# Kernel optimization log

Measured on AMD Instinct MI355X. Metric: run time of the kernel, lower is better.

## Reference

```python
import jax, jax.numpy as jnp
import numpy as np

N, E = 100000, 3200000
IN, HID, OUT, EDGE = 32, 32, 32, 8

def _lin(k, fi, fo):
    s = 1.0 / np.sqrt(fi)
    return jax.random.uniform(k, (fi, fo), jnp.float32, -s, s)

def setup_inputs() -> dict:
    key = jax.random.key(0)
    ks = jax.random.split(key, 12)
    return {
        "node_feat": jax.random.normal(ks[0], (N, IN), jnp.float32),
        "coord_feat": jax.random.normal(ks[1], (N, 3), jnp.float32),
        "edge_feat": jax.random.normal(ks[2], (E, EDGE), jnp.float32),
        "src": jax.random.randint(ks[3], (E,), 0, N, jnp.int32),
        "dst": jax.random.randint(ks[4], (E,), 0, N, jnp.int32),
        # edge MLP: Linear(2*IN+EDGE+1 -> HID), SiLU, Linear(HID -> HID), SiLU
        "We1": _lin(ks[5], 2 * IN + EDGE + 1, HID), "be1": jnp.zeros((HID,), jnp.float32),
        "We2": _lin(ks[6], HID, HID), "be2": jnp.zeros((HID,), jnp.float32),
        # node MLP: Linear(IN+HID -> HID), SiLU, Linear(HID -> OUT)
        "Wn1": _lin(ks[7], IN + HID, HID), "bn1": jnp.zeros((HID,), jnp.float32),
        "Wn2": _lin(ks[8], HID, OUT), "bn2": jnp.zeros((OUT,), jnp.float32),
        # coord MLP: Linear(HID -> HID), SiLU, Linear(HID -> 1, bias=False)
        "Wc1": _lin(ks[9], HID, HID), "bc1": jnp.zeros((HID,), jnp.float32),
        "Wc2": _lin(ks[10], HID, 1),
    }

def reference(node_feat, coord_feat, edge_feat, src, dst,
              We1, be1, We2, be2, Wn1, bn1, Wn2, bn2, Wc1, bc1, Wc2):
    silu = jax.nn.silu
    # per-edge coordinate difference and radial feature (DGL EGNNConv math)
    x_diff = coord_feat[src] - coord_feat[dst]                       # [E,3]
    radial = jnp.sum(x_diff * x_diff, axis=-1, keepdims=True)        # [E,1]
    x_diff = x_diff / (jnp.sqrt(radial) + 1e-30)                     # normalized
    # edge MLP on concat(src_h, dst_h, radial, edge_feat)
    f = jnp.concatenate([node_feat[src], node_feat[dst], radial, edge_feat], axis=-1)
    msg_h = silu(silu(f @ We1 + be1) @ We2 + be2)                    # [E,HID]
    # coordinate message (coord MLP scalar gate * normalized diff)
    msg_x = (silu(msg_h @ Wc1 + bc1) @ Wc2) * x_diff                 # [E,3]
    # aggregate: sum for h messages, mean for coord messages (at dst)
    h_neigh = jax.ops.segment_sum(msg_h, dst, num_segments=N)        # [N,HID]
    deg = jax.ops.segment_sum(jnp.ones((E, 1), msg_x.dtype), dst, num_segments=N)
    x_neigh = jax.ops.segment_sum(msg_x, dst, num_segments=N) / jnp.maximum(deg, 1.0)
    # node update
    h = silu(jnp.concatenate([node_feat, h_neigh], axis=-1) @ Wn1 + bn1) @ Wn2 + bn2
    x = coord_feat + x_neigh
    return h, x
```

## Files before the change

### kernel.cpp

```cpp
#include <hip/hip_runtime.h>
#include <math.h>

#define TIN   32
#define THID  32
#define TOUT  32
#define TEDGE 8
#define CHUNK 4
#define MAXDEG 64

typedef __attribute__((ext_vector_type(8))) short bf16x8;
typedef __attribute__((ext_vector_type(4))) float f32x4;

#define MFMA16(a, b, c) __builtin_amdgcn_mfma_f32_16x16x32_bf16((a), (b), (c), 0, 0, 0)

__device__ __forceinline__ unsigned int cvtpk(float lo, float hi) {
    unsigned int r;
    asm("v_cvt_pk_bf16_f32 %0, %1, %2" : "=v"(r) : "v"(lo), "v"(hi));
    return r;
}

__device__ __forceinline__ float silu_f(float x) {
    float e = __expf(-x);
    return x * __builtin_amdgcn_rcpf(1.0f + e);
}

union U4F { unsigned int u[4]; bf16x8 v; };
union U4Q { uint4 q; bf16x8 v; };

__device__ __forceinline__ bf16x8 pack8bf(const float* f) {
    U4F t;
    t.u[0] = cvtpk(f[0], f[1]);
    t.u[1] = cvtpk(f[2], f[3]);
    t.u[2] = cvtpk(f[4], f[5]);
    t.u[3] = cvtpk(f[6], f[7]);
    return t.v;
}

__device__ __forceinline__ bf16x8 load_wT(const float* __restrict__ W, int kbase, int ch, int Kreal) {
    float f[8];
    #pragma unroll
    for (int e = 0; e < 8; ++e) {
        int k = kbase + e;
        f[e] = (k < Kreal) ? W[k * 32 + ch] : 0.0f;
    }
    return pack8bf(f);
}

__device__ __forceinline__ bf16x8 load_wA12(const float* __restrict__ We1,
                                            const float* __restrict__ be1, int g, int ch) {
    float f[8];
    #pragma unroll
    for (int e = 0; e < 8; ++e) f[e] = 0.0f;
    if (g == 0) { f[0] = We1[64 * 32 + ch]; f[1] = be1[ch]; }
    else if (g == 1) {
        #pragma unroll
        for (int e = 0; e < 8; ++e) f[e] = We1[(65 + e) * 32 + ch];
    }
    return pack8bf(f);
}

__global__ __launch_bounds__(256) void conv_node_kernel(
    const float* __restrict__ nf, unsigned int* __restrict__ nb, int total )
{
    int i = blockIdx.x * 256 + threadIdx.x;
    int stride = gridDim.x * 256;
    for (; i < total; i += stride) {
        float2 v = reinterpret_cast<const float2*>(nf)[i];
        nb[i] = cvtpk(v.x, v.y);
    }
}

__global__ __launch_bounds__(256) void conv_coord_kernel(
    const float* __restrict__ c, float4* __restrict__ c4, int N)
{
    int i = blockIdx.x * 256 + threadIdx.x;
    int stride = gridDim.x * 256;
    for (; i < N; i += stride) {
        float4 v;
        v.x = c[3*(size_t)i+0]; v.y = c[3*(size_t)i+1]; v.z = c[3*(size_t)i+2]; v.w = 0.0f;
        c4[i] = v;
    }
}

__global__ __launch_bounds__(256) void record_rank_kernel(
    const int* __restrict__ src,
    const int* __restrict__ dst,
    const float* __restrict__ edge_feat,
    int* __restrict__ cnt,
    int* __restrict__ srcA,
    uint4* __restrict__ efA,
    int E)
{
    int e = blockIdx.x * 256 + threadIdx.x;
    if (e >= E) return;
    int d = dst[e];
    int rank = atomicAdd(&cnt[d], 1);
    if (rank >= MAXDEG) return;
    int slot = (d << 6) + rank;

    srcA[slot] = src[e];
    const float4* ep = reinterpret_cast<const float4*>(edge_feat + (size_t)e * TEDGE);
    float4 e0 = ep[0], e1 = ep[1];
    uint4 ef;
    ef.x = cvtpk(e0.x, e0.y);
    ef.y = cvtpk(e0.z, e0.w);
    ef.z = cvtpk(e1.x, e1.y);
    ef.w = cvtpk(e1.z, e1.w);
    efA[slot] = ef;
}

__global__ __launch_bounds__(256) void egnn_fused(
    const uint4* __restrict__ node_bf4,
    const float4* __restrict__ coord4,
    const int*  __restrict__ srcA,
    const uint4* __restrict__ efA,
    const int*  __restrict__ cnt,
    const float* __restrict__ We1,
    const float* __restrict__ be1,
    const float* __restrict__ We2,
    const float* __restrict__ be2,
    const float* __restrict__ Wc1,
    const float* __restrict__ bc1,
    const float* __restrict__ Wc2,
    float4* __restrict__ h_acc4,
    float4* __restrict__ xd4,
    int N)
{
    const int lane = threadIdx.x & 63;
    const int wid  = threadIdx.x >> 6;
    const int r    = lane & 15;
    const int g    = lane >> 4;

    bf16x8 A10[2], A11[2], A12[2], A2[2], A3[2];
    A10[0] = load_wT(We1,      8*g, r,      73);
    A10[1] = load_wT(We1,      8*g, 16 + r, 73);
    A11[0] = load_wT(We1, 32 + 8*g, r,      73);
    A11[1] = load_wT(We1, 32 + 8*g, 16 + r, 73);
    A12[0] = load_wA12(We1, be1, g, r);
    A12[1] = load_wA12(We1, be1, g, 16 + r);
    A2[0] = load_wT(We2, 8*g, r, 32);      A2[1] = load_wT(We2, 8*g, 16 + r, 32);
    A3[0] = load_wT(Wc1, 8*g, r, 32);      A3[1] = load_wT(Wc1, 8*g, 16 + r, 32);

    float be2v[8], bc1v[8], wc2v[8];
    #pragma unroll
    for (int h = 0; h < 2; ++h)
        #pragma unroll
        for (int q = 0; q < 4; ++q) {
            int ch = 16*h + 4*g + q;
            be2v[4*h+q] = be2[ch];
            bc1v[4*h+q] = bc1[ch];
            wc2v[4*h+q] = Wc2[ch];
        }

    const bool Hhi = ((g >> 1) & 1) != 0;
    const int  s0L = 32 * (g & 1) + r;
    const int  s1L = s0L + 16;

    int c0n = (blockIdx.x * 4 + wid) * CHUNK;

    for (int n = c0n; n < c0n + CHUNK && n < N; ++n) {
        int deg = cnt[n];
        int len = deg < MAXDEG ? deg : MAXDEG;
        int segbase = n << 6;

        U4Q Bd; Bd.q = node_bf4[(size_t)n * 4 + g];
        float4 cd = coord4[n];

        f32x4 z4 = {0.f,0.f,0.f,0.f};
        f32x4 dst0 = MFMA16(A11[0], Bd.v, z4);
        f32x4 dst1 = MFMA16(A11[1], Bd.v, z4);

        float ha0[4] = {0.f,0.f,0.f,0.f}, ha1[4] = {0.f,0.f,0.f,0.f};
        float xa0 = 0.f, xa1 = 0.f, xa2 = 0.f;

        for (int t = 0; t < len; t += 16) {
            int idx = t + r;
            bool valid = idx < len;
            int slot = segbase + (valid ? idx : 0);

            int srcv = srcA[slot];
            U4Q Bs; Bs.q = node_bf4[(size_t)srcv * 4 + g];

            float dx0 = 0.f, dx1 = 0.f, dx2 = 0.f;
            U4F Bk2;
            Bk2.u[0] = 0u; Bk2.u[1] = 0u; Bk2.u[2] = 0u; Bk2.u[3] = 0u;
            if (g == 0) {
                float4 cs = coord4[srcv];
                dx0 = cs.x - cd.x; dx1 = cs.y - cd.y; dx2 = cs.z - cd.z;
                float radial = dx0*dx0 + dx1*dx1 + dx2*dx2;
                float invn = __builtin_amdgcn_rcpf(sqrtf(radial) + 1e-30f);
                dx0 *= invn; dx1 *= invn; dx2 *= invn;
                Bk2.u[0] = cvtpk(radial, 1.0f);
            } else if (g == 1) {
                uint4 ef = efA[slot];
                Bk2.u[0] = ef.x; Bk2.u[1] = ef.y; Bk2.u[2] = ef.z; Bk2.u[3] = ef.w;
            }

            f32x4 acc0 = dst0, acc1 = dst1;
            acc0 = MFMA16(A10[0], Bs.v,   acc0);
            acc0 = MFMA16(A12[0], Bk2.v,  acc0);
            acc1 = MFMA16(A10[1], Bs.v,   acc1);
            acc1 = MFMA16(A12[1], Bk2.v,  acc1);

            unsigned int pk0 = cvtpk(silu_f(acc0[0]), silu_f(acc0[1]));
            unsigned int pk1 = cvtpk(silu_f(acc0[2]), silu_f(acc0[3]));
            unsigned int pk2 = cvtpk(silu_f(acc1[0]), silu_f(acc1[1]));
            unsigned int pk3 = cvtpk(silu_f(acc1[2]), silu_f(acc1[3]));

            unsigned int al0 = __shfl(pk0, s0L, 64), al1 = __shfl(pk1, s0L, 64);
            unsigned int ah0 = __shfl(pk2, s0L, 64), ah1 = __shfl(pk3, s0L, 64);
            unsigned int bl0 = __shfl(pk0, s1L, 64), bl1 = __shfl(pk1, s1L, 64);
            unsigned int bh0 = __shfl(pk2, s1L, 64), bh1 = __shfl(pk3, s1L, 64);
            U4F B2u;
            B2u.u[0] = Hhi ? ah0 : al0;  B2u.u[1] = Hhi ? ah1 : al1;
            B2u.u[2] = Hhi ? bh0 : bl0;  B2u.u[3] = Hhi ? bh1 : bl1;

            f32x4 m0, m1;
            #pragma unroll
            for (int q = 0; q < 4; ++q) { m0[q] = be2v[q]; m1[q] = be2v[4+q]; }
            m0 = MFMA16(A2[0], B2u.v, m0);
            m1 = MFMA16(A2[1], B2u.v, m1);

            float vm = valid ? 1.0f : 0.0f;
            float s00 = silu_f(m0[0]) * vm, s01 = silu_f(m0[1]) * vm;
            float s02 = silu_f(m0[2]) * vm, s03 = silu_f(m0[3]) * vm;
            float s10 = silu_f(m1[0]) * vm, s11 = silu_f(m1[1]) * vm;
            float s12 = silu_f(m1[2]) * vm, s13 = silu_f(m1[3]) * vm;

            ha0[0] += s00; ha0[1] += s01; ha0[2] += s02; ha0[3] += s03;
            ha1[0] += s10; ha1[1] += s11; ha1[2] += s12; ha1[3] += s13;

            unsigned int mpk0 = cvtpk(s00, s01);
            unsigned int mpk1 = cvtpk(s02, s03);
            unsigned int mpk2 = cvtpk(s10, s11);
            unsigned int mpk3 = cvtpk(s12, s13);

            unsigned int cl0 = __shfl(mpk0, s0L, 64), cl1 = __shfl(mpk1, s0L, 64);
            unsigned int ch0 = __shfl(mpk2, s0L, 64), ch1 = __shfl(mpk3, s0L, 64);
            unsigned int dl0 = __shfl(mpk0, s1L, 64), dl1 = __shfl(mpk1, s1L, 64);
            unsigned int dh0 = __shfl(mpk2, s1L, 64), dh1 = __shfl(mpk3, s1L, 64);
            U4F B3u;
            B3u.u[0] = Hhi ? ch0 : cl0;  B3u.u[1] = Hhi ? ch1 : cl1;
            B3u.u[2] = Hhi ? dh0 : dl0;  B3u.u[3] = Hhi ? dh1 : dl1;

            f32x4 c0, c1;
            #pragma unroll
            for (int q = 0; q < 4; ++q) { c0[q] = bc1v[q]; c1[q] = bc1v[4+q]; }
            c0 = MFMA16(A3[0], B3u.v, c0);
            c1 = MFMA16(A3[1], B3u.v, c1);

            float gp = 0.0f;
            #pragma unroll
            for (int q = 0; q < 4; ++q) {
                gp = fmaf(silu_f(c0[q]), wc2v[q],   gp);
                gp = fmaf(silu_f(c1[q]), wc2v[4+q], gp);
            }
            gp += __shfl_xor(gp, 16, 64);
            gp += __shfl_xor(gp, 32, 64);

            xa0 = fmaf(gp * vm, dx0, xa0);
            xa1 = fmaf(gp * vm, dx1, xa1);
            xa2 = fmaf(gp * vm, dx2, xa2);
        }

        #pragma unroll
        for (int off = 1; off < 16; off <<= 1) {
            #pragma unroll
            for (int q = 0; q < 4; ++q) {
                ha0[q] += __shfl_xor(ha0[q], off, 64);
                ha1[q] += __shfl_xor(ha1[q], off, 64);
            }
            xa0 += __shfl_xor(xa0, off, 64);
            xa1 += __shfl_xor(xa1, off, 64);
            xa2 += __shfl_xor(xa2, off, 64);
        }

        if (r == 0) {
            float4 v0; v0.x = ha0[0]; v0.y = ha0[1]; v0.z = ha0[2]; v0.w = ha0[3];
            float4 v1; v1.x = ha1[0]; v1.y = ha1[1]; v1.z = ha1[2]; v1.w = ha1[3];
            h_acc4[(size_t)n * 8 + g]     = v0;
            h_acc4[(size_t)n * 8 + 4 + g] = v1;
            if (g == 0) {
                float4 xv; xv.x = xa0; xv.y = xa1; xv.z = xa2; xv.w = (float)deg;
                xd4[n] = xv;
            }
        }
    }
}

__global__ __launch_bounds__(256) void ovf_fix_node(
    const float* __restrict__ node_feat,
    const float* __restrict__ coord,
    const float* __restrict__ edge_feat,
    const int* __restrict__ src,
    const int* __restrict__ dst,
    const int* __restrict__ cnt,
    const float* __restrict__ We1,
    const float* __restrict__ be1,
    const float* __restrict__ We2,
    const float* __restrict__ be2,
    const float* __restrict__ Wc1,
    const float* __restrict__ bc1,
    const float* __restrict__ Wc2,
    float* __restrict__ h_acc,
    float4* __restrict__ xd4,
    int N, int E)
{
    int n = blockIdx.x * 256 + threadIdx.x;
    if (n >= N) return;
    if (cnt[n] <= MAXDEG) return;

    float hsum[THID];
    #pragma unroll
    for (int j = 0; j < THID; ++j) hsum[j] = 0.f;
    float xs0 = 0.f, xs1 = 0.f, xs2 = 0.f;
    int degc = 0;
    for (int ee = 0; ee < E; ++ee) {
        if (dst[ee] != n) continue;
        ++degc;
        int ss = src[ee];
        float dx0 = coord[3*(size_t)ss+0] - coord[3*(size_t)n+0];
        float dx1 = coord[3*(size_t)ss+1] - coord[3*(size_t)n+1];
        float dx2 = coord[3*(size_t)ss+2] - coord[3*(size_t)n+2];
        float radial = dx0*dx0 + dx1*dx1 + dx2*dx2;
        float invn = 1.0f / (sqrtf(radial) + 1e-30f);
        dx0 *= invn; dx1 *= invn; dx2 *= invn;
        float f[73];
        for (int k = 0; k < 32; ++k) f[k] = node_feat[(size_t)ss*TIN + k];
        for (int k = 0; k < 32; ++k) f[32+k] = node_feat[(size_t)n*TIN + k];
        f[64] = radial;
        for (int k = 0; k < 8; ++k) f[65+k] = edge_feat[(size_t)ee*TEDGE + k];
        float a1[THID];
        for (int j = 0; j < THID; ++j) a1[j] = be1[j];
        for (int k = 0; k < 73; ++k) {
            float fk = f[k];
            for (int j = 0; j < THID; ++j) a1[j] = fmaf(fk, We1[k*THID + j], a1[j]);
        }
        for (int j = 0; j < THID; ++j) a1[j] = silu_f(a1[j]);
        float msg[THID];
        for (int j = 0; j < THID; ++j) msg[j] = be2[j];
        for (int k = 0; k < THID; ++k) {
            float fk = a1[k];
            for (int j = 0; j < THID; ++j) msg[j] = fmaf(fk, We2[k*THID + j], msg[j]);
        }
        for (int j = 0; j < THID; ++j) msg[j] = silu_f(msg[j]);
        float c1[THID];
        for (int j = 0; j < THID; ++j) c1[j] = bc1[j];
        for (int k = 0; k < THID; ++k) {
            float fk = msg[k];
            for (int j = 0; j < THID; ++j) c1[j] = fmaf(fk, Wc1[k*THID + j], c1[j]);
        }
        float gate = 0.0f;
        for (int j = 0; j < THID; ++j) gate = fmaf(silu_f(c1[j]), Wc2[j], gate);
        for (int j = 0; j < THID; ++j) hsum[j] += msg[j];
        xs0 += gate * dx0; xs1 += gate * dx1; xs2 += gate * dx2;
    }
    for (int j = 0; j < THID; ++j) h_acc[(size_t)n * THID + j] = hsum[j];
    float4 xv; xv.x = xs0; xv.y = xs1; xv.z = xs2; xv.w = (float)degc;
    xd4[n] = xv;
}

__global__ __launch_bounds__(256) void egnn_edge_atomic(
    const float* __restrict__ node_feat,
    const float* __restrict__ coord,
    const float* __restrict__ edge_feat,
    const int*   __restrict__ src,
    const int*   __restrict__ dst,
    const float* __restrict__ We1,
    const float* __restrict__ be1,
    const float* __restrict__ We2,
    const float* __restrict__ be2,
    const float* __restrict__ Wc1,
    const float* __restrict__ bc1,
    const float* __restrict__ Wc2,
    float* __restrict__ h_acc,
    float* __restrict__ x_acc,
    int E)
{
    int e = blockIdx.x * 256 + threadIdx.x;
    if (e >= E) return;
    int s = src[e];
    int d = dst[e];
    float dx0 = coord[3*(size_t)s+0] - coord[3*(size_t)d+0];
    float dx1 = coord[3*(size_t)s+1] - coord[3*(size_t)d+1];
    float dx2 = coord[3*(size_t)s+2] - coord[3*(size_t)d+2];
    float radial = dx0*dx0 + dx1*dx1 + dx2*dx2;
    float invn = 1.0f / (sqrtf(radial) + 1e-30f);
    dx0 *= invn; dx1 *= invn; dx2 *= invn;
    float f[73];
    #pragma unroll
    for (int i = 0; i < 32; ++i) f[i] = node_feat[(size_t)s*TIN + i];
    #pragma unroll
    for (int i = 0; i < 32; ++i) f[32+i] = node_feat[(size_t)d*TIN + i];
    f[64] = radial;
    #pragma unroll
    for (int i = 0; i < 8; ++i) f[65+i] = edge_feat[(size_t)e*TEDGE + i];
    float a1[THID];
    #pragma unroll
    for (int j = 0; j < THID; ++j) a1[j] = be1[j];
    for (int k = 0; k < 73; ++k) {
        float fk = f[k];
        #pragma unroll
        for (int j = 0; j < THID; ++j) a1[j] = fmaf(fk, We1[k*THID + j], a1[j]);
    }
    #pragma unroll
    for (int j = 0; j < THID; ++j) a1[j] = silu_f(a1[j]);
    float msg[THID];
    #pragma unroll
    for (int j = 0; j < THID; ++j) msg[j] = be2[j];
    for (int k = 0; k < THID; ++k) {
        float fk = a1[k];
        #pragma unroll
        for (int j = 0; j < THID; ++j) msg[j] = fmaf(fk, We2[k*THID + j], msg[j]);
    }
    #pragma unroll
    for (int j = 0; j < THID; ++j) msg[j] = silu_f(msg[j]);
    float c1[THID];
    #pragma unroll
    for (int j = 0; j < THID; ++j) c1[j] = bc1[j];
    for (int k = 0; k < THID; ++k) {
        float fk = msg[k];
        #pragma unroll
        for (int j = 0; j < THID; ++j) c1[j] = fmaf(fk, Wc1[k*THID + j], c1[j]);
    }
    float gate = 0.0f;
    #pragma unroll
    for (int j = 0; j < THID; ++j) gate = fmaf(silu_f(c1[j]), Wc2[j], gate);
    float* ha = h_acc + (size_t)d * THID;
    #pragma unroll
    for (int j = 0; j < THID; ++j) atomicAdd(ha + j, msg[j]);
    atomicAdd(x_acc + (size_t)d*4 + 0, gate * dx0);
    atomicAdd(x_acc + (size_t)d*4 + 1, gate * dx1);
    atomicAdd(x_acc + (size_t)d*4 + 2, gate * dx2);
    atomicAdd(x_acc + (size_t)d*4 + 3, 1.0f);
}

__global__ __launch_bounds__(256) void egnn_node(
    const float* __restrict__ node_feat,
    const float* __restrict__ coord,
    const float* __restrict__ Wn1,
    const float* __restrict__ bn1,
    const float* __restrict__ Wn2,
    const float* __restrict__ bn2,
    const float* __restrict__ h_acc,
    const float4* __restrict__ xd4,
    float* __restrict__ out_h,
    float* __restrict__ out_x,
    int N)
{
    int n = blockIdx.x * 256 + threadIdx.x;
    if (n >= N) return;

    float f2[2*TIN];
    {
        const float4* p = reinterpret_cast<const float4*>(node_feat + (size_t)n * TIN);
        #pragma unroll
        for (int i = 0; i < TIN/4; ++i) {
            float4 v = p[i];
            f2[4*i+0]=v.x; f2[4*i+1]=v.y; f2[4*i+2]=v.z; f2[4*i+3]=v.w;
        }
    }
    {
        const float4* p = reinterpret_cast<const float4*>(h_acc + (size_t)n * THID);
        #pragma unroll
        for (int i = 0; i < THID/4; ++i) {
            float4 v = p[i];
            f2[TIN+4*i+0]=v.x; f2[TIN+4*i+1]=v.y; f2[TIN+4*i+2]=v.z; f2[TIN+4*i+3]=v.w;
        }
    }

    float a[THID];
    #pragma unroll
    for (int j = 0; j < THID; ++j) a[j] = bn1[j];
    #pragma unroll
    for (int k = 0; k < 2*TIN; ++k) {
        float fk = f2[k];
        #pragma unroll
        for (int j = 0; j < THID; ++j) a[j] = fmaf(fk, Wn1[k*THID + j], a[j]);
    }
    #pragma unroll
    for (int j = 0; j < THID; ++j) a[j] = silu_f(a[j]);

    float h[TOUT];
    #pragma unroll
    for (int j = 0; j < TOUT; ++j) h[j] = bn2[j];
    #pragma unroll
    for (int k = 0; k < THID; ++k) {
        float fk = a[k];
        #pragma unroll
        for (int j = 0; j < TOUT; ++j) h[j] = fmaf(fk, Wn2[k*TOUT + j], h[j]);
    }

    float4* po = reinterpret_cast<float4*>(out_h + (size_t)n * TOUT);
    #pragma unroll
    for (int i = 0; i < TOUT/4; ++i) {
        float4 v; v.x=h[4*i+0]; v.y=h[4*i+1]; v.z=h[4*i+2]; v.w=h[4*i+3];
        po[i] = v;
    }

    float4 xv = xd4[n];
    float dg = fmaxf(xv.w, 1.0f);
    float inv = __builtin_amdgcn_rcpf(dg);
    out_x[(size_t)n*3+0] = coord[(size_t)n*3+0] + xv.x * inv;
    out_x[(size_t)n*3+1] = coord[(size_t)n*3+1] + xv.y * inv;
    out_x[(size_t)n*3+2] = coord[(size_t)n*3+2] + xv.z * inv;
}

extern "C" void kernel_launch(void* const* d_in, const int* in_sizes, int n_in,
                              void* d_out, int out_size, void* d_ws, size_t ws_size,
                              hipStream_t stream) {
    const float* node_feat = (const float*)d_in[0];
    const float* coord     = (const float*)d_in[1];
    const float* edge_feat = (const float*)d_in[2];
    const int*   src       = (const int*)d_in[3];
    const int*   dst       = (const int*)d_in[4];
    const float* We1 = (const float*)d_in[5];
    const float* be1 = (const float*)d_in[6];
    const float* We2 = (const float*)d_in[7];
    const float* be2 = (const float*)d_in[8];
    const float* Wn1 = (const float*)d_in[9];
    const float* bn1 = (const float*)d_in[10];
    const float* Wn2 = (const float*)d_in[11];
    const float* bn2 = (const float*)d_in[12];
    const float* Wc1 = (const float*)d_in[13];
    const float* bc1 = (const float*)d_in[14];
    const float* Wc2 = (const float*)d_in[15];

    int N = in_sizes[0] / TIN;
    int E = in_sizes[3];

    float* out_h = (float*)d_out;
    float* out_x = out_h + (size_t)N * TOUT;

    uint4*        efA     = (uint4*)d_ws;
    float4*       coord4  = (float4*)(efA + ((size_t)N << 6));
    float4*       xd4     = coord4 + N;
    float*        h_acc   = (float*)(xd4 + N);
    unsigned int* node_bf = (unsigned int*)(h_acc + (size_t)N * THID);
    int*          srcA    = (int*)(node_bf + (size_t)N * 16);
    int*          cnt     = srcA + ((size_t)N << 6);
    size_t need = (size_t)((char*)(cnt + N + 1) - (char*)d_ws);

    if (need <= ws_size) {
        conv_node_kernel<<<2048, 256, 0, stream>>>(node_feat, node_bf, N * 16);
        conv_coord_kernel<<<(N + 255) / 256, 256, 0, stream>>>(coord, coord4, N);
        hipMemsetAsync(cnt, 0, (size_t)(N + 1) * 4, stream);
        record_rank_kernel<<<(E + 255) / 256, 256, 0, stream>>>(
            src, dst, edge_feat, cnt, srcA, efA, E);
        int nchunks = (N + CHUNK - 1) / CHUNK;
        egnn_fused<<<(nchunks + 3) / 4, 256, 0, stream>>>(
            (const uint4*)node_bf, coord4, srcA, efA, cnt,
            We1, be1, We2, be2, Wc1, bc1, Wc2,
            (float4*)h_acc, xd4, N);
        ovf_fix_node<<<(N + 255) / 256, 256, 0, stream>>>(
            node_feat, coord, edge_feat, src, dst, cnt,
            We1, be1, We2, be2, Wc1, bc1, Wc2, h_acc, xd4, N, E);
        egnn_node<<<(N + 255) / 256, 256, 0, stream>>>(
            node_feat, coord, Wn1, bn1, Wn2, bn2,
            h_acc, xd4, out_h, out_x, N);
    } else {
        float* fh_acc = (float*)d_ws;
        float* fx_acc = fh_acc + (size_t)N * THID;
        hipMemsetAsync(d_ws, 0, sizeof(float) * (size_t)N * (THID + 4), stream);
        egnn_edge_atomic<<<(E + 255) / 256, 256, 0, stream>>>(
            node_feat, coord, edge_feat, src, dst,
            We1, be1, We2, be2, Wc1, bc1, Wc2,
            fh_acc, fx_acc, E);
        egnn_node<<<(N + 255) / 256, 256, 0, stream>>>(
            node_feat, coord, Wn1, bn1, Wn2, bn2,
            fh_acc, (const float4*)fx_acc, out_h, out_x, N);
    }
}
```

Baseline: 520.0 us.

## Precompute per-edge geometry in rank kernel and pack into 32-byte edge records

After: 476.4 us. 8.4% less time.

```diff
diff --git a/kernel.cpp b/kernel.cpp
--- a/kernel.cpp
+++ b/kernel.cpp
@@ -23,6 +23,9 @@
     float e = __expf(-x);
     return x * __builtin_amdgcn_rcpf(1.0f + e);
 }
+
+__device__ __forceinline__ float bflo(unsigned int u) { return __uint_as_float(u << 16); }
+__device__ __forceinline__ float bfhi(unsigned int u) { return __uint_as_float(u & 0xFFFF0000u); }
 
 union U4F { unsigned int u[4]; bf16x8 v; };
 union U4Q { uint4 q; bf16x8 v; };
@@ -51,10 +54,10 @@
     float f[8];
     #pragma unroll
     for (int e = 0; e < 8; ++e) f[e] = 0.0f;
-    if (g == 0) { f[0] = We1[64 * 32 + ch]; f[1] = be1[ch]; }
+    if (g == 0) { f[0] = We1[72 * 32 + ch]; f[1] = be1[ch]; }
     else if (g == 1) {
         #pragma unroll
-        for (int e = 0; e < 8; ++e) f[e] = We1[(65 + e) * 32 + ch];
+        for (int e = 0; e < 8; ++e) f[e] = We1[(64 + e) * 32 + ch];
     }
     return pack8bf(f);
 }
@@ -85,35 +88,45 @@
 __global__ __launch_bounds__(256) void record_rank_kernel(
     const int* __restrict__ src,
     const int* __restrict__ dst,
+    const float4* __restrict__ coord4,
     const float* __restrict__ edge_feat,
     int* __restrict__ cnt,
-    int* __restrict__ srcA,
-    uint4* __restrict__ efA,
+    uint4* __restrict__ recs,
     int E)
 {
     int e = blockIdx.x * 256 + threadIdx.x;
     if (e >= E) return;
-    int d = dst[e];
+    int s = src[e], d = dst[e];
     int rank = atomicAdd(&cnt[d], 1);
     if (rank >= MAXDEG) return;
-    int slot = (d << 6) + rank;
-
-    srcA[slot] = src[e];
+
+    float4 cs = coord4[s];
+    float4 cd = coord4[d];
+    float dx0 = cs.x - cd.x, dx1 = cs.y - cd.y, dx2 = cs.z - cd.z;
+    float radial = dx0*dx0 + dx1*dx1 + dx2*dx2;
+    float invn = __builtin_amdgcn_rcpf(sqrtf(radial) + 1e-30f);
+    dx0 *= invn; dx1 *= invn; dx2 *= invn;
+
     const float4* ep = reinterpret_cast<const float4*>(edge_feat + (size_t)e * TEDGE);
     float4 e0 = ep[0], e1 = ep[1];
-    uint4 ef;
-    ef.x = cvtpk(e0.x, e0.y);
-    ef.y = cvtpk(e0.z, e0.w);
-    ef.z = cvtpk(e1.x, e1.y);
-    ef.w = cvtpk(e1.z, e1.w);
-    efA[slot] = ef;
+
+    size_t slot = ((size_t)d << 6) + rank;
+    uint4 r0, r1;
+    r0.x = (unsigned int)s;
+    r0.y = cvtpk(dx0, dx1);
+    r0.z = cvtpk(dx2, e1.w);
+    r0.w = 0u;
+    r1.x = cvtpk(radial, e0.x);
+    r1.y = cvtpk(e0.y, e0.z);
+    r1.z = cvtpk(e0.w, e1.x);
+    r1.w = cvtpk(e1.y, e1.z);
+    recs[2*slot + 0] = r0;
+    recs[2*slot + 1] = r1;
 }
 
 __global__ __launch_bounds__(256) void egnn_fused(
     const uint4* __restrict__ node_bf4,
-    const float4* __restrict__ coord4,
-    const int*  __restrict__ srcA,
-    const uint4* __restrict__ efA,
+    const uint4* __restrict__ recs,
     const int*  __restrict__ cnt,
     const float* __restrict__ We1,
     const float* __restrict__ be1,
@@ -161,10 +174,9 @@
     for (int n = c0n; n < c0n + CHUNK && n < N; ++n) {
         int deg = cnt[n];
         int len = deg < MAXDEG ? deg : MAXDEG;
-        int segbase = n << 6;
+        size_t segbase = ((size_t)n << 6);
 
         U4Q Bd; Bd.q = node_bf4[(size_t)n * 4 + g];
-        float4 cd = coord4[n];
 
         f32x4 z4 = {0.f,0.f,0.f,0.f};
         f32x4 dst0 = MFMA16(A11[0], Bd.v, z4);
@@ -176,24 +188,19 @@
         for (int t = 0; t < len; t += 16) {
             int idx = t + r;
             bool valid = idx < len;
-            int slot = segbase + (valid ? idx : 0);
-
-            int srcv = srcA[slot];
+            size_t slot = segbase + (valid ? idx : 0);
+
+            uint4 rc = recs[2*slot + (g & 1)];
+            int srcv = __shfl((int)rc.x, r, 64);
+
             U4Q Bs; Bs.q = node_bf4[(size_t)srcv * 4 + g];
 
-            float dx0 = 0.f, dx1 = 0.f, dx2 = 0.f;
             U4F Bk2;
             Bk2.u[0] = 0u; Bk2.u[1] = 0u; Bk2.u[2] = 0u; Bk2.u[3] = 0u;
             if (g == 0) {
-                float4 cs = coord4[srcv];
-                dx0 = cs.x - cd.x; dx1 = cs.y - cd.y; dx2 = cs.z - cd.z;
-                float radial = dx0*dx0 + dx1*dx1 + dx2*dx2;
-                float invn = __builtin_amdgcn_rcpf(sqrtf(radial) + 1e-30f);
-                dx0 *= invn; dx1 *= invn; dx2 *= invn;
-                Bk2.u[0] = cvtpk(radial, 1.0f);
+                Bk2.u[0] = (rc.z >> 16) | 0x3F800000u;
             } else if (g == 1) {
-                uint4 ef = efA[slot];
-                Bk2.u[0] = ef.x; Bk2.u[1] = ef.y; Bk2.u[2] = ef.z; Bk2.u[3] = ef.w;
+                Bk2.u[0] = rc.x; Bk2.u[1] = rc.y; Bk2.u[2] = rc.z; Bk2.u[3] = rc.w;
             }
 
             f32x4 acc0 = dst0, acc1 = dst1;
@@ -258,9 +265,10 @@
             gp += __shfl_xor(gp, 16, 64);
             gp += __shfl_xor(gp, 32, 64);
 
-            xa0 = fmaf(gp * vm, dx0, xa0);
-            xa1 = fmaf(gp * vm, dx1, xa1);
-            xa2 = fmaf(gp * vm, dx2, xa2);
+            float xd0 = bflo(rc.y), xd1 = bfhi(rc.y), xd2 = bflo(rc.z);
+            xa0 = fmaf(gp * vm, xd0, xa0);
+            xa1 = fmaf(gp * vm, xd1, xa1);
+            xa2 = fmaf(gp * vm, xd2, xa2);
         }
 
         #pragma unroll
@@ -532,13 +540,12 @@
     float* out_h = (float*)d_out;
     float* out_x = out_h + (size_t)N * TOUT;
 
-    uint4*        efA     = (uint4*)d_ws;
-    float4*       coord4  = (float4*)(efA + ((size_t)N << 6));
-    float4*       xd4     = coord4 + N;
-    float*        h_acc   = (float*)(xd4 + N);
-    unsigned int* node_bf = (unsigned int*)(h_acc + (size_t)N * THID);
-    int*          srcA    = (int*)(node_bf + (size_t)N * 16);
-    int*          cnt     = srcA + ((size_t)N << 6);
+    uint4*        recs    = (uint4*)d_ws;
+    unsigned int* node_bf = (unsigned int*)(recs + ((size_t)N << 6) * 2);
+    float4*       coord4  = (float4*)(node_bf + (size_t)N * 16);
+    float*        h_acc   = (float*)(coord4 + N);
+    float4*       xd4     = (float4*)(h_acc + (size_t)N * THID);
+    int*          cnt     = (int*)(xd4 + N);
     size_t need = (size_t)((char*)(cnt + N + 1) - (char*)d_ws);
 
     if (need <= ws_size) {
@@ -546,10 +553,10 @@
         conv_coord_kernel<<<(N + 255) / 256, 256, 0, stream>>>(coord, coord4, N);
         hipMemsetAsync(cnt, 0, (size_t)(N + 1) * 4, stream);
         record_rank_kernel<<<(E + 255) / 256, 256, 0, stream>>>(
-            src, dst, edge_feat, cnt, srcA, efA, E);
+            src, dst, coord4, edge_feat, cnt, recs, E);
         int nchunks = (N + CHUNK - 1) / CHUNK;
         egnn_fused<<<(nchunks + 3) / 4, 256, 0, stream>>>(
-            (const uint4*)node_bf, coord4, srcA, efA, cnt,
+            (const uint4*)node_bf, recs, cnt,
             We1, be1, We2, be2, Wc1, bc1, Wc2,
             (float4*)h_acc, xd4, N);
         ovf_fix_node<<<(N + 255) / 256, 256, 0, stream>>>(
```
